# Kernel optimization log

Hardware: AMD Instinct MI355X
Metric: run time of the kernel (lower is better)

Reference implementation:

```python
import jax, jax.numpy as jnp
import numpy as np

E = 64          # embedding_dim
H = 2 * E       # GRU hidden = input size = 128
ATT_HID = 36    # activation-unit MLP hidden


def _gru_scan(x, Wih, Whh, bih, bhh):
    """Standard (PyTorch-convention) GRU over x:[B,T,D] -> outputs [B,T,H]."""
    B = x.shape[0]
    gx = jnp.einsum('btd,gd->btg', x, Wih) + bih        # [B,T,3H], precompute input gates
    gx = jnp.swapaxes(gx, 0, 1)                          # [T,B,3H]
    h0 = jnp.zeros((B, H), x.dtype)

    def step(h, g):
        gh = h @ Whh.T + bhh                             # [B,3H]
        xr, xz, xn = jnp.split(g, 3, axis=-1)
        hr, hz, hn = jnp.split(gh, 3, axis=-1)
        r = jax.nn.sigmoid(xr + hr)
        z = jax.nn.sigmoid(xz + hz)
        n = jnp.tanh(xn + r * hn)
        h = (1.0 - z) * n + z * h
        return h, h

    _, hs = jax.lax.scan(step, h0, gx)                   # [T,B,H]
    return jnp.swapaxes(hs, 0, 1)                        # [B,T,H]


def _augru_scan(x, att, Wih, Whh, bih, bhh):
    """AUGRU: attention score scales the update gate. x:[B,T,H], att:[B,T]."""
    B = x.shape[0]
    gx = jnp.einsum('btd,gd->btg', x, Wih) + bih         # [B,T,3H]
    gx = jnp.swapaxes(gx, 0, 1)                          # [T,B,3H]
    a = jnp.swapaxes(att, 0, 1)[..., None]               # [T,B,1]
    h0 = jnp.zeros((B, H), x.dtype)

    def step(h, inp):
        g, at = inp
        gh = h @ Whh.T + bhh
        xr, xz, xn = jnp.split(g, 3, axis=-1)
        hr, hz, hn = jnp.split(gh, 3, axis=-1)
        r = jax.nn.sigmoid(xr + hr)
        u = jax.nn.sigmoid(xz + hz) * at                 # attention-modulated update gate
        n = jnp.tanh(xn + r * hn)
        h = (1.0 - u) * h + u * n
        return h, h

    _, hs = jax.lax.scan(step, h0, (gx, a))
    return jnp.swapaxes(hs, 0, 1)                        # [B,T,H]


def _attention_scores(query, hist, mask, W1, b1, W2, b2):
    """DIN activation unit: MLP over [q, h, q-h, q*h] -> masked softmax over T."""
    q = jnp.broadcast_to(query[:, None, :], hist.shape)  # [B,T,H]
    feat = jnp.concatenate([q, hist, q - hist, q * hist], axis=-1)  # [B,T,4H]
    hidden = jax.nn.sigmoid(jnp.einsum('btf,uf->btu', feat, W1) + b1)
    logits = (jnp.einsum('btu,ou->bto', hidden, W2) + b2)[..., 0]    # [B,T]
    logits = jnp.where(mask > 0, logits, -1e9)
    return jax.nn.softmax(logits, axis=-1)


def setup_inputs() -> dict:
    key = jax.random.key(0)
    ks = jax.random.split(key, 12)
    B, T = 1024, 200
    query_ad = jax.random.normal(ks[0], (B, H), jnp.float32)
    user_behavior = jax.random.normal(ks[1], (B, T, H), jnp.float32)
    lengths = jax.random.randint(ks[2], (B,), 1, T + 1)
    mask = (jnp.arange(T)[None, :] < lengths[:, None]).astype(jnp.int32)
    s = 1.0 / np.sqrt(H)
    p = {
        'gru_Wih': jax.random.uniform(ks[3], (3 * H, H), jnp.float32, -s, s),
        'gru_Whh': jax.random.uniform(ks[4], (3 * H, H), jnp.float32, -s, s),
        'gru_bih': jnp.zeros((3 * H,), jnp.float32),
        'gru_bhh': jnp.zeros((3 * H,), jnp.float32),
        'att_W1': jax.random.normal(ks[5], (ATT_HID, 4 * H), jnp.float32) * 0.05,
        'att_b1': jnp.zeros((ATT_HID,), jnp.float32),
        'att_W2': jax.random.normal(ks[6], (1, ATT_HID), jnp.float32) * 0.05,
        'att_b2': jnp.zeros((1,), jnp.float32),
        'augru_Wih': jax.random.uniform(ks[7], (3 * H, H), jnp.float32, -s, s),
        'augru_Whh': jax.random.uniform(ks[8], (3 * H, H), jnp.float32, -s, s),
        'augru_bih': jnp.zeros((3 * H,), jnp.float32),
        'augru_bhh': jnp.zeros((3 * H,), jnp.float32),
    }
    return dict(query_ad=query_ad, user_behavior=user_behavior, mask=mask, **p)


def reference(query_ad, user_behavior, mask,
              gru_Wih, gru_Whh, gru_bih, gru_bhh,
              att_W1, att_b1, att_W2, att_b2,
              augru_Wih, augru_Whh, augru_bih, augru_bhh):
    hist = _gru_scan(user_behavior, gru_Wih, gru_Whh, gru_bih, gru_bhh)       # [B,T,H]
    att = _attention_scores(query_ad, hist, mask, att_W1, att_b1, att_W2, att_b2)  # [B,T]
    out = _augru_scan(hist, att, augru_Wih, augru_Whh, augru_bih, augru_bhh)  # [B,T,H]
    lengths = jnp.sum(mask, axis=1)                                            # [B]
    B = out.shape[0]
    return out[jnp.arange(B), lengths - 1]                                     # [B,H]
```

## Files before the change

### kernel.cpp

```cpp
#include <hip/hip_runtime.h>

typedef _Float16 f16;
typedef _Float16 f16x8 __attribute__((ext_vector_type(8)));
typedef _Float16 f16x4 __attribute__((ext_vector_type(4)));
typedef float    f32x4 __attribute__((ext_vector_type(4)));

#define H  128
#define G3 384
#define AH 36
#define PADW 136

__device__ __forceinline__ float sigmoidf_(float x){
  return __builtin_amdgcn_rcpf(1.f + __expf(-x));
}
__device__ __forceinline__ float tanhf_(float x){
  return fmaf(2.f, __builtin_amdgcn_rcpf(1.f + __expf(-2.f*x)), -1.f);
}

__device__ __forceinline__ void lds_sync(){
  asm volatile("s_waitcnt lgkmcnt(0)" ::: "memory");
  __builtin_amdgcn_s_barrier();
  asm volatile("" ::: "memory");
}

__global__ void prep_weights(const float* __restrict__ a, const float* __restrict__ b,
                             const float* __restrict__ c, const float* __restrict__ d,
                             f16* __restrict__ dst)
{
  int i = blockIdx.x * 256 + threadIdx.x;
  if (i >= 4 * G3 * H) return;
  int m = i / (G3 * H), j = i % (G3 * H);
  const float* s = (m == 0) ? a : (m == 1) ? b : (m == 2) ? c : d;
  dst[i] = (f16)s[j];
}

__global__ void prep_len(const int* __restrict__ mask, int* __restrict__ len, int T, int B)
{
  int b = blockIdx.x * 256 + threadIdx.x;
  if (b >= B) return;
  int s = 0;
  for (int t = 0; t < T; ++t) s += (mask[(size_t)b * T + t] > 0);
  len[b] = s;
}

template<bool AUG>
__global__ __launch_bounds__(512)
__attribute__((amdgpu_waves_per_eu(2, 2)))
void scan_kernel(const float* __restrict__ xf32,
                 const f16*   __restrict__ xf16,
                 const f16*   __restrict__ Wih,
                 const f16*   __restrict__ Whh,
                 const float* __restrict__ bih,
                 const float* __restrict__ bhh,
                 const float* __restrict__ att,
                 const int*   __restrict__ len,
                 f16*         __restrict__ histo,
                 float*       __restrict__ outp,
                 int T)
{
  __shared__ f16  xs[2][16 * PADW];
  __shared__ f16  hs[2][16 * PADW];

  const int tid = threadIdx.x;
  const int w   = tid >> 6;
  const int l   = tid & 63;
  const int l16 = l & 15;
  const int lhi = l >> 4;
  const int b0  = blockIdx.x * 16;
  const int colb = w * 16;
  const int c4   = colb + lhi * 4;
  const int srow = tid >> 5, cc = tid & 31;

  f16x8 wih[3][4], whh[3][4];
  #pragma unroll
  for (int g = 0; g < 3; ++g)
    #pragma unroll
    for (int q = 0; q < 4; ++q) {
      int off = (g * H + colb + l16) * H + q * 32 + lhi * 8;
      wih[g][q] = *(const f16x8*)(Wih + off);
      whh[g][q] = *(const f16x8*)(Whh + off);
    }
  #pragma unroll
  for (int g = 0; g < 3; ++g)
    #pragma unroll
    for (int q = 0; q < 4; ++q)
      asm volatile("" : "+v"(wih[g][q]), "+v"(whh[g][q]));

  f32x4 bRs = *(const f32x4*)(bih + c4);
  { f32x4 t2 = *(const f32x4*)(bhh + c4);     bRs += t2; }
  f32x4 bZs = *(const f32x4*)(bih + H + c4);
  { f32x4 t2 = *(const f32x4*)(bhh + H + c4); bZs += t2; }
  f32x4 bXn = *(const f32x4*)(bih + 2*H + c4);
  f32x4 bHn = *(const f32x4*)(bhh + 2*H + c4);

  float hold[4] = {0.f, 0.f, 0.f, 0.f};
  int len_l = 0;
  if (AUG) len_l = len[b0 + l16];

  const f16* xrd0 = &xs[0][l16 * PADW + lhi * 8];
  const f16* xrd1 = &xs[1][l16 * PADW + lhi * 8];
  const f16* hrd0 = &hs[0][l16 * PADW + lhi * 8];
  const f16* hrd1 = &hs[1][l16 * PADW + lhi * 8];
  f16* hwr0 = &hs[0][l16 * PADW + c4];
  f16* hwr1 = &hs[1][l16 * PADW + c4];
  f16* xst0 = &xs[0][srow * PADW + cc * 4];
  f16* xst1 = &xs[1][srow * PADW + cc * 4];

  const float* pxA32 = xf32 ? (xf32 + ((size_t)(b0 + srow) * T) * H + cc * 4) : nullptr;
  const f16*   pxA16 = xf16 ? (xf16 + ((size_t)(b0 + srow) * T) * H + cc * 4) : nullptr;
  const float* attB  = AUG ? (att + (size_t)(b0 + l16) * T) : nullptr;
  f16*         histp = (!AUG && histo) ? (histo + ((size_t)(b0 + l16) * T) * H + c4) : nullptr;
  float*       outpp = AUG ? (outp + (size_t)(b0 + l16) * H + c4) : nullptr;

  {
    f16x4 z4 = {(f16)0, (f16)0, (f16)0, (f16)0};
    *(f16x4*)(&hs[0][srow * PADW + cc * 4]) = z4;
    if (AUG) {
      f16x4 v = *(const f16x4*)(pxA16);
      *(f16x4*)xst0 = v;
    } else {
      f32x4 v = *(const f32x4*)(pxA32);
      f16x4 h4 = {(f16)v.x, (f16)v.y, (f16)v.z, (f16)v.w};
      *(f16x4*)xst0 = h4;
    }
  }
  f32x4 Pa32 = {0,0,0,0}, Pb32 = {0,0,0,0};
  f16x4 Pa16 = {(f16)0,(f16)0,(f16)0,(f16)0}, Pb16 = Pa16;
  float Aa = 0.f, Ab = 0.f;
  if (AUG) {
    Pa16 = *(const f16x4*)(pxA16 + H);
    Aa = attB[0];
    if (T > 1) Ab = attB[1];
  } else {
    Pa32 = *(const f32x4*)(pxA32 + H);
  }
  const float* pxE32 = pxA32 ? pxA32 + 2 * H : nullptr;
  const float* pxO32 = pxA32 ? pxA32 + 3 * H : nullptr;
  const f16*   pxE16 = pxA16 ? pxA16 + 2 * H : nullptr;
  const f16*   pxO16 = pxA16 ? pxA16 + 3 * H : nullptr;
  lds_sync();

#define STEP(targ_, XRD, HRD, HWRN, XSTN, PW32, PL32, PW16, PL16, AW, PXP32, PXP16) \
  {                                                                            \
    const int t5_  = (targ_);                                                  \
    float at_ = 0.f;                                                           \
    if (AUG) at_ = AW;                                                         \
    if (t5_ + 2 < T) {                                                         \
      if (AUG) {                                                               \
        PL16 = *(const f16x4*)(PXP16);  PXP16 += 2 * H;                        \
        AW = attB[t5_ + 2];                                                    \
      } else {                                                                 \
        PL32 = *(const f32x4*)(PXP32);  PXP32 += 2 * H;                        \
      }                                                                        \
    }                                                                          \
    f16x8 xb[4], hb[4];                                                        \
    _Pragma("unroll")                                                          \
    for (int q = 0; q < 4; ++q) {                                              \
      xb[q] = *(const f16x8*)(XRD + q * 32);                                   \
      hb[q] = *(const f16x8*)(HRD + q * 32);                                   \
    }                                                                          \
    f32x4 aZx = bZs, aZh = {0,0,0,0};                                          \
    _Pragma("unroll")                                                          \
    for (int q = 0; q < 4; ++q) {                                              \
      aZx = __builtin_amdgcn_mfma_f32_16x16x32_f16(wih[1][q], xb[q], aZx,0,0,0); \
      aZh = __builtin_amdgcn_mfma_f32_16x16x32_f16(whh[1][q], hb[q], aZh,0,0,0); \
    }                                                                          \
    f32x4 aRx = bRs, aRh = {0,0,0,0};                                          \
    _Pragma("unroll")                                                          \
    for (int q = 0; q < 4; ++q) {                                              \
      aRx = __builtin_amdgcn_mfma_f32_16x16x32_f16(wih[0][q], xb[q], aRx,0,0,0); \
      aRh = __builtin_amdgcn_mfma_f32_16x16x32_f16(whh[0][q], hb[q], aRh,0,0,0); \
    }                                                                          \
    float z_[4];                                                               \
    _Pragma("unroll")                                                          \
    for (int i = 0; i < 4; ++i) z_[i] = sigmoidf_(aZx[i] + aZh[i]);            \
    f32x4 aNx = bXn, aNh = bHn;                                                \
    _Pragma("unroll")                                                          \
    for (int q = 0; q < 4; ++q) {                                              \
      aNx = __builtin_amdgcn_mfma_f32_16x16x32_f16(wih[2][q], xb[q], aNx,0,0,0); \
      aNh = __builtin_amdgcn_mfma_f32_16x16x32_f16(whh[2][q], hb[q], aNh,0,0,0); \
    }                                                                          \
    float r_[4];                                                               \
    _Pragma("unroll")                                                          \
    for (int i = 0; i < 4; ++i) r_[i] = sigmoidf_(aRx[i] + aRh[i]);            \
    float hn_[4];                                                              \
    _Pragma("unroll")                                                          \
    for (int i = 0; i < 4; ++i) {                                              \
      float n = tanhf_(aNx[i] + r_[i] * aNh[i]);                               \
      float h;                                                                 \
      if (AUG) { float u = z_[i] * at_; h = hold[i] + u * (n - hold[i]); }     \
      else     { h = n + z_[i] * (hold[i] - n); }                              \
      hold[i] = h; hn_[i] = h;                                                 \
    }                                                                          \
    f16x4 hv = {(f16)hn_[0], (f16)hn_[1], (f16)hn_[2], (f16)hn_[3]};           \
    *(f16x4*)(HWRN) = hv;                                                      \
    if (!AUG) {                                                                \
      *(f16x4*)histp = hv;  histp += H;                                        \
    } else {                                                                   \
      if (t5_ == len_l - 1) {                                                  \
        f32x4 ov = {hn_[0], hn_[1], hn_[2], hn_[3]};                           \
        *(f32x4*)outpp = ov;                                                   \
      }                                                                        \
    }                                                                          \
    if (t5_ + 1 < T) {                                                         \
      if (AUG) {                                                               \
        *(f16x4*)(XSTN) = PW16;                                                \
      } else {                                                                 \
        f16x4 s4 = {(f16)PW32.x, (f16)PW32.y, (f16)PW32.z, (f16)PW32.w};       \
        *(f16x4*)(XSTN) = s4;                                                  \
      }                                                                        \
    }                                                                          \
    lds_sync();                                                                \
  }

  for (int t = 0; t < T; t += 2) {
    STEP(t,     xrd0, hrd0, hwr1, xst1, Pa32, Pb32, Pa16, Pb16, Aa, pxE32, pxE16)
    STEP(t + 1, xrd1, hrd1, hwr0, xst0, Pb32, Pa32, Pb16, Pa16, Ab, pxO32, pxO16)
  }
#undef STEP
}

__global__ __launch_bounds__(256)
void attn_kernel(const float* __restrict__ query,
                 const f16*   __restrict__ hist,
                 const int*   __restrict__ mask,
                 const float* __restrict__ W1, const float* __restrict__ b1,
                 const float* __restrict__ W2, const float* __restrict__ b2,
                 float* __restrict__ attv, int T)
{
  __shared__ float qs[H];
  __shared__ f16   WqH[48 * PADW];
  __shared__ float qcp[48], w2p[48];
  __shared__ float logitsS[224];
  __shared__ float red[256];

  const int tid = threadIdx.x, b = blockIdx.x;
  const int w = tid >> 6, l = tid & 63, l16 = l & 15, lhi = l >> 4;

  if (tid < H) qs[tid] = query[b * H + tid];
  if (tid < 48) w2p[tid] = (tid < AH) ? W2[tid] : 0.f;
  __syncthreads();

  for (int i = tid; i < 48 * H; i += 256) {
    int u = i >> 7, k = i & (H - 1);
    float v = 0.f;
    if (u < AH) {
      const float* r = W1 + u * 4 * H;
      v = r[H + k] - r[2*H + k] + qs[k] * r[3*H + k];
    }
    WqH[u * PADW + k] = (f16)v;
  }
  if (tid < 48) {
    float s = 0.f;
    if (tid < AH) {
      const float* r = W1 + tid * 4 * H;
      s = b1[tid];
      for (int k = 0; k < H; ++k) s += qs[k] * (r[k] + r[2*H + k]);
    }
    qcp[tid] = s;
  }
  __syncthreads();

  const f32x4 qcv0 = *(const f32x4*)&qcp[lhi*4];
  const f32x4 qcv1 = *(const f32x4*)&qcp[16 + lhi*4];
  const f32x4 qcv2 = *(const f32x4*)&qcp[32 + lhi*4];
  const f32x4 w2v0 = *(const f32x4*)&w2p[lhi*4];
  const f32x4 w2v1 = *(const f32x4*)&w2p[16 + lhi*4];
  const f32x4 w2v2 = *(const f32x4*)&w2p[32 + lhi*4];

  const int NMT = (T + 15) >> 4;
  for (int mt = w; mt < NMT; mt += 4) {
    const int t0 = mt * 16;
    f16x8 hbf[4];
    #pragma unroll
    for (int q = 0; q < 4; ++q)
      hbf[q] = *(const f16x8*)(hist + ((size_t)b*T + t0 + l16)*H + q*32 + lhi*8);
    f32x4 d0 = {0,0,0,0}, d1 = {0,0,0,0}, d2 = {0,0,0,0};
    #pragma unroll
    for (int q = 0; q < 4; ++q) {
      f16x8 wq0 = *(const f16x8*)(&WqH[ l16       * PADW + q*32 + lhi*8]);
      f16x8 wq1 = *(const f16x8*)(&WqH[(16 + l16) * PADW + q*32 + lhi*8]);
      f16x8 wq2 = *(const f16x8*)(&WqH[(32 + l16) * PADW + q*32 + lhi*8]);
      d0 = __builtin_amdgcn_mfma_f32_16x16x32_f16(wq0, hbf[q], d0, 0,0,0);
      d1 = __builtin_amdgcn_mfma_f32_16x16x32_f16(wq1, hbf[q], d1, 0,0,0);
      d2 = __builtin_amdgcn_mfma_f32_16x16x32_f16(wq2, hbf[q], d2, 0,0,0);
    }
    float p = 0.f;
    #pragma unroll
    for (int i = 0; i < 4; ++i) {
      p += w2v0[i] * sigmoidf_(d0[i] + qcv0[i]);
      p += w2v1[i] * sigmoidf_(d1[i] + qcv1[i]);
      p += w2v2[i] * sigmoidf_(d2[i] + qcv2[i]);
    }
    p += __shfl_xor(p, 16, 64);
    p += __shfl_xor(p, 32, 64);
    if (lhi == 0) logitsS[t0 + l16] = p;
  }
  __syncthreads();

  const int t = tid;
  float logit = -1e30f; int mk = 0;
  if (t < T) {
    mk = mask[(size_t)b*T + t];
    logit = (mk > 0) ? (logitsS[t] + b2[0]) : -1e30f;
  }
  red[tid] = logit; __syncthreads();
  for (int s = 128; s > 0; s >>= 1) { if (tid < s) red[tid] = fmaxf(red[tid], red[tid+s]); __syncthreads(); }
  float mx = red[0]; __syncthreads();
  float ev = (t < T && mk > 0) ? __expf(logit - mx) : 0.f;
  red[tid] = ev; __syncthreads();
  for (int s = 128; s > 0; s >>= 1) { if (tid < s) red[tid] += red[tid+s]; __syncthreads(); }
  float sm = red[0];
  if (t < T) attv[(size_t)b*T + t] = ev * __builtin_amdgcn_rcpf(sm);
}

extern "C" void kernel_launch(void* const* d_in, const int* in_sizes, int n_in,
                              void* d_out, int out_size, void* d_ws, size_t ws_size,
                              hipStream_t stream)
{
  const float* query = (const float*)d_in[0];
  const float* ub    = (const float*)d_in[1];
  const int*   mask  = (const int*)d_in[2];
  const float* gWih  = (const float*)d_in[3];
  const float* gWhh  = (const float*)d_in[4];
  const float* gbih  = (const float*)d_in[5];
  const float* gbhh  = (const float*)d_in[6];
  const float* aW1   = (const float*)d_in[7];
  const float* ab1   = (const float*)d_in[8];
  const float* aW2   = (const float*)d_in[9];
  const float* ab2   = (const float*)d_in[10];
  const float* uWih  = (const float*)d_in[11];
  const float* uWhh  = (const float*)d_in[12];
  const float* ubih  = (const float*)d_in[13];
  const float* ubhh  = (const float*)d_in[14];

  const int B = in_sizes[0] / H;
  const int T = in_sizes[1] / in_sizes[0];

  char*  ws   = (char*)d_ws;
  f16*   wf   = (f16*)ws;
  int*   lenp = (int*)(ws + 393216);
  float* attb = (float*)(ws + 397312);
  f16*   hist = (f16*)(ws + 397312 + (size_t)B * 200 * 4);

  prep_weights<<<(4 * G3 * H + 255) / 256, 256, 0, stream>>>(gWih, gWhh, uWih, uWhh, wf);
  prep_len<<<(B + 255) / 256, 256, 0, stream>>>(mask, lenp, T, B);

  scan_kernel<false><<<B / 16, 512, 0, stream>>>(
      ub, (const f16*)nullptr, wf, wf + G3 * H, gbih, gbhh,
      (const float*)nullptr, (const int*)nullptr, hist, (float*)nullptr, T);

  attn_kernel<<<B, 256, 0, stream>>>(query, hist, mask, aW1, ab1, aW2, ab2, attb, T);

  scan_kernel<true><<<B / 16, 512, 0, stream>>>(
      (const float*)nullptr, hist, wf + 2 * G3 * H, wf + 3 * G3 * H, ubih, ubhh,
      attb, lenp, (f16*)nullptr, (float*)d_out, T);
}
```

Before: 377.8 us.

## Process two 16-row batch tiles per block in GRU scans for ILP

Each scan block now handles 32 batch rows as two independent 16-row tiles, A and B. Their MFMA chains and gate math interleave within every timestep, so the latency of one tile's dependent recurrence can be hidden behind the other's work. The r and z accumulators now sum the input and hidden products into a single register, which cuts accumulator count. The grid shrinks by half, which risks underfilling the GPU when B is small, and the extra live registers could spill.

Result: slower. 653.0 us (+72.8%).

```diff
diff --git a/kernel.cpp b/kernel.cpp
--- a/kernel.cpp
+++ b/kernel.cpp
@@ -58,15 +58,15 @@
                  float*       __restrict__ outp,
                  int T)
 {
-  __shared__ f16  xs[2][16 * PADW];
-  __shared__ f16  hs[2][16 * PADW];
+  __shared__ f16 xsA[2][16 * PADW], hsA[2][16 * PADW];
+  __shared__ f16 xsB[2][16 * PADW], hsB[2][16 * PADW];
 
   const int tid = threadIdx.x;
   const int w   = tid >> 6;
   const int l   = tid & 63;
   const int l16 = l & 15;
   const int lhi = l >> 4;
-  const int b0  = blockIdx.x * 16;
+  const int b0  = blockIdx.x * 32;
   const int colb = w * 16;
   const int c4   = colb + lhi * 4;
   const int srow = tid >> 5, cc = tid & 31;
@@ -93,129 +93,189 @@
   f32x4 bXn = *(const f32x4*)(bih + 2*H + c4);
   f32x4 bHn = *(const f32x4*)(bhh + 2*H + c4);
 
-  float hold[4] = {0.f, 0.f, 0.f, 0.f};
-  int len_l = 0;
-  if (AUG) len_l = len[b0 + l16];
-
-  const f16* xrd0 = &xs[0][l16 * PADW + lhi * 8];
-  const f16* xrd1 = &xs[1][l16 * PADW + lhi * 8];
-  const f16* hrd0 = &hs[0][l16 * PADW + lhi * 8];
-  const f16* hrd1 = &hs[1][l16 * PADW + lhi * 8];
-  f16* hwr0 = &hs[0][l16 * PADW + c4];
-  f16* hwr1 = &hs[1][l16 * PADW + c4];
-  f16* xst0 = &xs[0][srow * PADW + cc * 4];
-  f16* xst1 = &xs[1][srow * PADW + cc * 4];
-
-  const float* pxA32 = xf32 ? (xf32 + ((size_t)(b0 + srow) * T) * H + cc * 4) : nullptr;
-  const f16*   pxA16 = xf16 ? (xf16 + ((size_t)(b0 + srow) * T) * H + cc * 4) : nullptr;
-  const float* attB  = AUG ? (att + (size_t)(b0 + l16) * T) : nullptr;
-  f16*         histp = (!AUG && histo) ? (histo + ((size_t)(b0 + l16) * T) * H + c4) : nullptr;
-  float*       outpp = AUG ? (outp + (size_t)(b0 + l16) * H + c4) : nullptr;
+  float holdA[4] = {0.f,0.f,0.f,0.f}, holdB[4] = {0.f,0.f,0.f,0.f};
+  int len_lA = 0, len_lB = 0;
+  if (AUG) { len_lA = len[b0 + l16]; len_lB = len[b0 + 16 + l16]; }
+
+  const f16* xrdA0 = &xsA[0][l16*PADW + lhi*8];
+  const f16* xrdA1 = &xsA[1][l16*PADW + lhi*8];
+  const f16* hrdA0 = &hsA[0][l16*PADW + lhi*8];
+  const f16* hrdA1 = &hsA[1][l16*PADW + lhi*8];
+  f16* hwrA0 = &hsA[0][l16*PADW + c4];
+  f16* hwrA1 = &hsA[1][l16*PADW + c4];
+  f16* xstA0 = &xsA[0][srow*PADW + cc*4];
+  f16* xstA1 = &xsA[1][srow*PADW + cc*4];
+  const f16* xrdB0 = &xsB[0][l16*PADW + lhi*8];
+  const f16* xrdB1 = &xsB[1][l16*PADW + lhi*8];
+  const f16* hrdB0 = &hsB[0][l16*PADW + lhi*8];
+  const f16* hrdB1 = &hsB[1][l16*PADW + lhi*8];
+  f16* hwrB0 = &hsB[0][l16*PADW + c4];
+  f16* hwrB1 = &hsB[1][l16*PADW + c4];
+  f16* xstB0 = &xsB[0][srow*PADW + cc*4];
+  f16* xstB1 = &xsB[1][srow*PADW + cc*4];
+
+  const float* pxA32_A = xf32 ? (xf32 + ((size_t)(b0 + srow)      * T) * H + cc*4) : nullptr;
+  const float* pxA32_B = xf32 ? (xf32 + ((size_t)(b0 + 16 + srow) * T) * H + cc*4) : nullptr;
+  const f16*   pxA16_A = xf16 ? (xf16 + ((size_t)(b0 + srow)      * T) * H + cc*4) : nullptr;
+  const f16*   pxA16_B = xf16 ? (xf16 + ((size_t)(b0 + 16 + srow) * T) * H + cc*4) : nullptr;
+  const float* attBA = AUG ? (att + (size_t)(b0 + l16) * T)      : nullptr;
+  const float* attBB = AUG ? (att + (size_t)(b0 + 16 + l16) * T) : nullptr;
+  f16* histpA = (!AUG && histo) ? (histo + ((size_t)(b0 + l16)      * T) * H + c4) : nullptr;
+  f16* histpB = (!AUG && histo) ? (histo + ((size_t)(b0 + 16 + l16) * T) * H + c4) : nullptr;
+  float* outppA = AUG ? (outp + (size_t)(b0 + l16)      * H + c4) : nullptr;
+  float* outppB = AUG ? (outp + (size_t)(b0 + 16 + l16) * H + c4) : nullptr;
 
   {
-    f16x4 z4 = {(f16)0, (f16)0, (f16)0, (f16)0};
-    *(f16x4*)(&hs[0][srow * PADW + cc * 4]) = z4;
+    f16x4 z4 = {(f16)0,(f16)0,(f16)0,(f16)0};
+    *(f16x4*)(&hsA[0][srow*PADW + cc*4]) = z4;
+    *(f16x4*)(&hsB[0][srow*PADW + cc*4]) = z4;
     if (AUG) {
-      f16x4 v = *(const f16x4*)(pxA16);
-      *(f16x4*)xst0 = v;
+      *(f16x4*)xstA0 = *(const f16x4*)(pxA16_A);
+      *(f16x4*)xstB0 = *(const f16x4*)(pxA16_B);
     } else {
-      f32x4 v = *(const f32x4*)(pxA32);
-      f16x4 h4 = {(f16)v.x, (f16)v.y, (f16)v.z, (f16)v.w};
-      *(f16x4*)xst0 = h4;
-    }
-  }
-  f32x4 Pa32 = {0,0,0,0}, Pb32 = {0,0,0,0};
-  f16x4 Pa16 = {(f16)0,(f16)0,(f16)0,(f16)0}, Pb16 = Pa16;
-  float Aa = 0.f, Ab = 0.f;
+      f32x4 va = *(const f32x4*)(pxA32_A);
+      f32x4 vb = *(const f32x4*)(pxA32_B);
+      f16x4 ha = {(f16)va.x,(f16)va.y,(f16)va.z,(f16)va.w};
+      f16x4 hb = {(f16)vb.x,(f16)vb.y,(f16)vb.z,(f16)vb.w};
+      *(f16x4*)xstA0 = ha;
+      *(f16x4*)xstB0 = hb;
+    }
+  }
+  f32x4 Pa32A={0,0,0,0}, Pb32A={0,0,0,0}, Pa32B={0,0,0,0}, Pb32B={0,0,0,0};
+  f16x4 Pa16A={(f16)0,(f16)0,(f16)0,(f16)0}, Pb16A=Pa16A, Pa16B=Pa16A, Pb16B=Pa16A;
+  float AaA=0.f, AbA=0.f, AaB=0.f, AbB=0.f;
   if (AUG) {
-    Pa16 = *(const f16x4*)(pxA16 + H);
-    Aa = attB[0];
-    if (T > 1) Ab = attB[1];
+    if (T > 1) { Pa16A = *(const f16x4*)(pxA16_A + H); Pa16B = *(const f16x4*)(pxA16_B + H); }
+    AaA = attBA[0]; AaB = attBB[0];
+    if (T > 1) { AbA = attBA[1]; AbB = attBB[1]; }
   } else {
-    Pa32 = *(const f32x4*)(pxA32 + H);
-  }
-  const float* pxE32 = pxA32 ? pxA32 + 2 * H : nullptr;
-  const float* pxO32 = pxA32 ? pxA32 + 3 * H : nullptr;
-  const f16*   pxE16 = pxA16 ? pxA16 + 2 * H : nullptr;
-  const f16*   pxO16 = pxA16 ? pxA16 + 3 * H : nullptr;
+    if (T > 1) { Pa32A = *(const f32x4*)(pxA32_A + H); Pa32B = *(const f32x4*)(pxA32_B + H); }
+  }
+  const float* pxEA32 = pxA32_A ? pxA32_A + 2*H : nullptr;
+  const float* pxOA32 = pxA32_A ? pxA32_A + 3*H : nullptr;
+  const float* pxEB32 = pxA32_B ? pxA32_B + 2*H : nullptr;
+  const float* pxOB32 = pxA32_B ? pxA32_B + 3*H : nullptr;
+  const f16*   pxEA16 = pxA16_A ? pxA16_A + 2*H : nullptr;
+  const f16*   pxOA16 = pxA16_A ? pxA16_A + 3*H : nullptr;
+  const f16*   pxEB16 = pxA16_B ? pxA16_B + 2*H : nullptr;
+  const f16*   pxOB16 = pxA16_B ? pxA16_B + 3*H : nullptr;
   lds_sync();
 
-#define STEP(targ_, XRD, HRD, HWRN, XSTN, PW32, PL32, PW16, PL16, AW, PXP32, PXP16) \
+#define STEP(t5v, XRDA_, HRDA_, HWRA_, XSTA_, XRDB_, HRDB_, HWRB_, XSTB_,      \
+             PW32A, PL32A, PW16A, PL16A, AWA_,                                 \
+             PW32B, PL32B, PW16B, PL16B, AWB_, PXA32, PXA16, PXB32, PXB16)     \
   {                                                                            \
-    const int t5_  = (targ_);                                                  \
-    float at_ = 0.f;                                                           \
-    if (AUG) at_ = AW;                                                         \
+    const int t5_ = (t5v);                                                     \
+    float atA_ = 0.f, atB_ = 0.f;                                              \
+    if (AUG) { atA_ = AWA_; atB_ = AWB_; }                                     \
     if (t5_ + 2 < T) {                                                         \
       if (AUG) {                                                               \
-        PL16 = *(const f16x4*)(PXP16);  PXP16 += 2 * H;                        \
-        AW = attB[t5_ + 2];                                                    \
+        PL16A = *(const f16x4*)(PXA16);  PXA16 += 2*H;                         \
+        PL16B = *(const f16x4*)(PXB16);  PXB16 += 2*H;                         \
+        AWA_ = attBA[t5_ + 2];  AWB_ = attBB[t5_ + 2];                         \
       } else {                                                                 \
-        PL32 = *(const f32x4*)(PXP32);  PXP32 += 2 * H;                        \
+        PL32A = *(const f32x4*)(PXA32);  PXA32 += 2*H;                         \
+        PL32B = *(const f32x4*)(PXB32);  PXB32 += 2*H;                         \
       }                                                                        \
     }                                                                          \
-    f16x8 xb[4], hb[4];                                                        \
-    _Pragma("unroll")                                                          \
-    for (int q = 0; q < 4; ++q) {                                              \
-      xb[q] = *(const f16x8*)(XRD + q * 32);                                   \
-      hb[q] = *(const f16x8*)(HRD + q * 32);                                   \
-    }                                                                          \
-    f32x4 aZx = bZs, aZh = {0,0,0,0};                                          \
-    _Pragma("unroll")                                                          \
-    for (int q = 0; q < 4; ++q) {                                              \
-      aZx = __builtin_amdgcn_mfma_f32_16x16x32_f16(wih[1][q], xb[q], aZx,0,0,0); \
-      aZh = __builtin_amdgcn_mfma_f32_16x16x32_f16(whh[1][q], hb[q], aZh,0,0,0); \
-    }                                                                          \
-    f32x4 aRx = bRs, aRh = {0,0,0,0};                                          \
-    _Pragma("unroll")                                                          \
-    for (int q = 0; q < 4; ++q) {                                              \
-      aRx = __builtin_amdgcn_mfma_f32_16x16x32_f16(wih[0][q], xb[q], aRx,0,0,0); \
-      aRh = __builtin_amdgcn_mfma_f32_16x16x32_f16(whh[0][q], hb[q], aRh,0,0,0); \
-    }                                                                          \
-    float z_[4];                                                               \
-    _Pragma("unroll")                                                          \
-    for (int i = 0; i < 4; ++i) z_[i] = sigmoidf_(aZx[i] + aZh[i]);            \
-    f32x4 aNx = bXn, aNh = bHn;                                                \
-    _Pragma("unroll")                                                          \
-    for (int q = 0; q < 4; ++q) {                                              \
-      aNx = __builtin_amdgcn_mfma_f32_16x16x32_f16(wih[2][q], xb[q], aNx,0,0,0); \
-      aNh = __builtin_amdgcn_mfma_f32_16x16x32_f16(whh[2][q], hb[q], aNh,0,0,0); \
-    }                                                                          \
-    float r_[4];                                                               \
-    _Pragma("unroll")                                                          \
-    for (int i = 0; i < 4; ++i) r_[i] = sigmoidf_(aRx[i] + aRh[i]);            \
-    float hn_[4];                                                              \
+    f16x8 xba_[4], hba_[4];                                                    \
+    _Pragma("unroll")                                                          \
+    for (int q = 0; q < 4; ++q) {                                              \
+      xba_[q] = *(const f16x8*)(XRDA_ + q*32);                                 \
+      hba_[q] = *(const f16x8*)(HRDA_ + q*32);                                 \
+    }                                                                          \
+    f32x4 aRA = bRs, aZA = bZs, aXnA = bXn, aHnA = bHn;                        \
+    _Pragma("unroll")                                                          \
+    for (int q = 0; q < 4; ++q) {                                              \
+      aRA  = __builtin_amdgcn_mfma_f32_16x16x32_f16(wih[0][q], xba_[q], aRA, 0,0,0); \
+      aZA  = __builtin_amdgcn_mfma_f32_16x16x32_f16(wih[1][q], xba_[q], aZA, 0,0,0); \
+      aXnA = __builtin_amdgcn_mfma_f32_16x16x32_f16(wih[2][q], xba_[q], aXnA,0,0,0); \
+      aHnA = __builtin_amdgcn_mfma_f32_16x16x32_f16(whh[2][q], hba_[q], aHnA,0,0,0); \
+    }                                                                          \
+    _Pragma("unroll")                                                          \
+    for (int q = 0; q < 4; ++q) {                                              \
+      aRA  = __builtin_amdgcn_mfma_f32_16x16x32_f16(whh[0][q], hba_[q], aRA, 0,0,0); \
+      aZA  = __builtin_amdgcn_mfma_f32_16x16x32_f16(whh[1][q], hba_[q], aZA, 0,0,0); \
+    }                                                                          \
+    f16x8 xbb_[4], hbb_[4];                                                    \
+    _Pragma("unroll")                                                          \
+    for (int q = 0; q < 4; ++q) {                                              \
+      xbb_[q] = *(const f16x8*)(XRDB_ + q*32);                                 \
+      hbb_[q] = *(const f16x8*)(HRDB_ + q*32);                                 \
+    }                                                                          \
+    f32x4 aRB = bRs, aZB = bZs, aXnB = bXn, aHnB = bHn;                        \
+    _Pragma("unroll")                                                          \
+    for (int q = 0; q < 4; ++q) {                                              \
+      aRB  = __builtin_amdgcn_mfma_f32_16x16x32_f16(wih[0][q], xbb_[q], aRB, 0,0,0); \
+      aZB  = __builtin_amdgcn_mfma_f32_16x16x32_f16(wih[1][q], xbb_[q], aZB, 0,0,0); \
+      aXnB = __builtin_amdgcn_mfma_f32_16x16x32_f16(wih[2][q], xbb_[q], aXnB,0,0,0); \
+      aHnB = __builtin_amdgcn_mfma_f32_16x16x32_f16(whh[2][q], hbb_[q], aHnB,0,0,0); \
+    }                                                                          \
+    _Pragma("unroll")                                                          \
+    for (int q = 0; q < 4; ++q) {                                              \
+      aRB  = __builtin_amdgcn_mfma_f32_16x16x32_f16(whh[0][q], hbb_[q], aRB, 0,0,0); \
+      aZB  = __builtin_amdgcn_mfma_f32_16x16x32_f16(whh[1][q], hbb_[q], aZB, 0,0,0); \
+    }                                                                          \
+    float hnA_[4];                                                             \
     _Pragma("unroll")                                                          \
     for (int i = 0; i < 4; ++i) {                                              \
-      float n = tanhf_(aNx[i] + r_[i] * aNh[i]);                               \
+      float r = sigmoidf_(aRA[i]);                                             \
+      float z = sigmoidf_(aZA[i]);                                             \
+      float n = tanhf_(aXnA[i] + r * aHnA[i]);                                 \
       float h;                                                                 \
-      if (AUG) { float u = z_[i] * at_; h = hold[i] + u * (n - hold[i]); }     \
-      else     { h = n + z_[i] * (hold[i] - n); }                              \
-      hold[i] = h; hn_[i] = h;                                                 \
-    }                                                                          \
-    f16x4 hv = {(f16)hn_[0], (f16)hn_[1], (f16)hn_[2], (f16)hn_[3]};           \
-    *(f16x4*)(HWRN) = hv;                                                      \
+      if (AUG) { float u = z * atA_; h = holdA[i] + u * (n - holdA[i]); }      \
+      else     { h = n + z * (holdA[i] - n); }                                 \
+      holdA[i] = h; hnA_[i] = h;                                               \
+    }                                                                          \
+    float hnB_[4];                                                             \
+    _Pragma("unroll")                                                          \
+    for (int i = 0; i < 4; ++i) {                                              \
+      float r = sigmoidf_(aRB[i]);                                             \
+      float z = sigmoidf_(aZB[i]);                                             \
+      float n = tanhf_(aXnB[i] + r * aHnB[i]);                                 \
+      float h;                                                                 \
+      if (AUG) { float u = z * atB_; h = holdB[i] + u * (n - holdB[i]); }      \
+      else     { h = n + z * (holdB[i] - n); }                                 \
+      holdB[i] = h; hnB_[i] = h;                                               \
+    }                                                                          \
+    f16x4 hvA = {(f16)hnA_[0],(f16)hnA_[1],(f16)hnA_[2],(f16)hnA_[3]};         \
+    f16x4 hvB = {(f16)hnB_[0],(f16)hnB_[1],(f16)hnB_[2],(f16)hnB_[3]};         \
+    *(f16x4*)(HWRA_) = hvA;                                                    \
+    *(f16x4*)(HWRB_) = hvB;                                                    \
     if (!AUG) {                                                                \
-      *(f16x4*)histp = hv;  histp += H;                                        \
+      *(f16x4*)histpA = hvA;  histpA += H;                                     \
+      *(f16x4*)histpB = hvB;  histpB += H;                                     \
     } else {                                                                   \
-      if (t5_ == len_l - 1) {                                                  \
-        f32x4 ov = {hn_[0], hn_[1], hn_[2], hn_[3]};                           \
-        *(f32x4*)outpp = ov;                                                   \
+      if (t5_ == len_lA - 1) {                                                 \
+        f32x4 ov = {hnA_[0],hnA_[1],hnA_[2],hnA_[3]};                          \
+        *(f32x4*)outppA = ov;                                                  \
+      }                                                                        \
+      if (t5_ == len_lB - 1) {                                                 \
+        f32x4 ov = {hnB_[0],hnB_[1],hnB_[2],hnB_[3]};                          \
+        *(f32x4*)outppB = ov;                                                  \
       }                                                                        \
     }                                                                          \
     if (t5_ + 1 < T) {                                                         \
       if (AUG) {                                                               \
-        *(f16x4*)(XSTN) = PW16;                                                \
+        *(f16x4*)(XSTA_) = PW16A;                                              \
+        *(f16x4*)(XSTB_) = PW16B;                                              \
       } else {                                                                 \
-        f16x4 s4 = {(f16)PW32.x, (f16)PW32.y, (f16)PW32.z, (f16)PW32.w};       \
-        *(f16x4*)(XSTN) = s4;                                                  \
+        f16x4 sa_ = {(f16)PW32A.x,(f16)PW32A.y,(f16)PW32A.z,(f16)PW32A.w};     \
+        f16x4 sb_ = {(f16)PW32B.x,(f16)PW32B.y,(f16)PW32B.z,(f16)PW32B.w};     \
+        *(f16x4*)(XSTA_) = sa_;                                                \
+        *(f16x4*)(XSTB_) = sb_;                                                \
       }                                                                        \
     }                                                                          \
     lds_sync();                                                                \
   }
 
   for (int t = 0; t < T; t += 2) {
-    STEP(t,     xrd0, hrd0, hwr1, xst1, Pa32, Pb32, Pa16, Pb16, Aa, pxE32, pxE16)
-    STEP(t + 1, xrd1, hrd1, hwr0, xst0, Pb32, Pa32, Pb16, Pa16, Ab, pxO32, pxO16)
+    STEP(t,     xrdA0, hrdA0, hwrA1, xstA1, xrdB0, hrdB0, hwrB1, xstB1,
+         Pa32A, Pb32A, Pa16A, Pb16A, AaA,
+         Pa32B, Pb32B, Pa16B, Pb16B, AaB, pxEA32, pxEA16, pxEB32, pxEB16)
+    STEP(t + 1, xrdA1, hrdA1, hwrA0, xstA0, xrdB1, hrdB1, hwrB0, xstB0,
+         Pb32A, Pa32A, Pb16A, Pa16A, AbA,
+         Pb32B, Pa32B, Pb16B, Pa16B, AbB, pxOA32, pxOA16, pxOB32, pxOB16)
   }
 #undef STEP
 }
@@ -346,13 +406,13 @@
   prep_weights<<<(4 * G3 * H + 255) / 256, 256, 0, stream>>>(gWih, gWhh, uWih, uWhh, wf);
   prep_len<<<(B + 255) / 256, 256, 0, stream>>>(mask, lenp, T, B);
 
-  scan_kernel<false><<<B / 16, 512, 0, stream>>>(
+  scan_kernel<false><<<B / 32, 512, 0, stream>>>(
       ub, (const f16*)nullptr, wf, wf + G3 * H, gbih, gbhh,
       (const float*)nullptr, (const int*)nullptr, hist, (float*)nullptr, T);
 
   attn_kernel<<<B, 256, 0, stream>>>(query, hist, mask, aW1, ab1, aW2, ab2, attb, T);
 
-  scan_kernel<true><<<B / 16, 512, 0, stream>>>(
+  scan_kernel<true><<<B / 32, 512, 0, stream>>>(
       (const float*)nullptr, hist, wf + 2 * G3 * H, wf + 3 * G3 * H, ubih, ubhh,
       attb, lenp, (f16*)nullptr, (float*)d_out, T);
 }
```
